# Kernel tuning notes

Hardware: AMD Instinct MI355X
Metric: run time of the kernel (lower is better)

## Reference

```python
import jax, jax.numpy as jnp
import numpy as np

# dims: B batch, N nodes, E edges, C=dim_in, W=window_len, D=embed_dim, O=dim_out, K=link_len, NB=bootstrap count
B, N, E, C, W, D, O, K, NB = 16, 2000, 3000, 17, 12, 16, 256, 3, 3


def setup_inputs() -> dict:
    key = jax.random.key(0)
    ks = jax.random.split(key, 20)
    return {
        "x": jax.random.normal(ks[0], (B, N, C), jnp.float32),
        "x_window": jax.random.normal(ks[1], (B, W, N, 1), jnp.float32),
        "node_embeddings": jax.random.normal(ks[2], (N, D), jnp.float32) * 0.1,
        "fixed_adj": 0,
        "adj": jax.random.normal(ks[3], (N, N), jnp.float32),
        "stay_cost": 1,
        "jump_cost": 1,
        "ZFC_input": jax.random.normal(ks[4], (B, O // 8), jnp.float32),
        "hodge_Laplacian": jax.random.normal(ks[5], (E, E), jnp.float32) * 0.02,
        "x_e_window": jax.random.normal(ks[6], (B, W, E, 1), jnp.float32),
        "incidence_matrix": jax.random.normal(ks[7], (N, E), jnp.float32) * 0.02,
        "weights_pool": jax.random.normal(ks[8], (D, K, C, O // 4), jnp.float32) * 0.05,
        "window_weights_supra": jax.random.normal(ks[9], (D, 1, O // 8), jnp.float32) * 0.05,
        "window_weights_temporal": jax.random.normal(ks[10], (D, 1, O // 2), jnp.float32) * 0.05,
        "bias_pool": jax.random.normal(ks[11], (D, O), jnp.float32) * 0.05,
        "T_param": jax.random.normal(ks[12], (W,), jnp.float32) * 0.1,
        "lin_w": jax.random.normal(ks[13], (1, 1), jnp.float32),
        "lin_b": jax.random.normal(ks[14], (1,), jnp.float32),
        "gnn_w": jax.random.normal(ks[15], (N, N), jnp.float32) * 0.02,
        "gnn_b": jnp.zeros((N,), jnp.float32),
        "bootstrap_idx": jnp.sort(jax.random.randint(ks[16], (NB,), 0, W)),
    }


def _forward(x, x_window, ne, fixed_adj, adj, stay_cost, jump_cost, ZFC_input,
             hodge, x_e_window, inc, wp, wws_p, wwt_p, bp, Tp, lin_w, lin_b,
             gnn_w, gnn_b, bidx):
    n = ne.shape[0]
    e = hodge.shape[0]
    b = x.shape[0]
    nb = bidx.shape[0]

    # adaptive transition matrix S (diag filled with stay_cost after relu)
    S0 = jax.nn.relu(ne @ ne.T)
    ii = jnp.arange(n)
    S0 = S0.at[ii, ii].set(jnp.float32(stay_cost))
    if fixed_adj:  # static Python bool branch
        S = adj * jnp.exp(S0)
    else:
        S = jax.nn.softmax(S0, axis=1)
    # faithful to torch broadcasting: column j divided by row-sum of row j
    S = S / jnp.sum(S, axis=1)

    # diffusion support power series: [I, S, S@S, ...]
    sup = [jnp.eye(n, dtype=S.dtype), S]
    for _ in range(2, K):
        sup.append(S @ sup[-1])
    supports = jnp.stack(sup, axis=0)  # (K, N, N)

    # supra-Laplacian: hodge on diagonal blocks, jump_cost*I on strict upper blocks
    supra = (jnp.kron(jnp.eye(nb, dtype=hodge.dtype), hodge)
             + jnp.kron(jnp.triu(jnp.ones((nb, nb), hodge.dtype), 1),
                        jnp.float32(jump_cost) * jnp.eye(e, dtype=hodge.dtype)))  # (nb*E, nb*E)

    # adaptive weights/bias from node embeddings
    weights = jnp.einsum('nd,dkio->nkio', ne, wp)   # (N, K, C, O/4)
    bias = ne @ bp                                   # (N, O)

    # graph diffusion branch
    x_s = jnp.einsum('knm,bmc->bknc', supports, x).transpose(0, 2, 1, 3)  # (B,N,K,C)
    x_sconv = jnp.einsum('bnki,nkio->bno', x_s, weights)                   # (B,N,O/4)

    # supra / hypergraph branch
    wws = jnp.einsum('nd,dio->nio', ne, wws_p)                 # (N,1,O/8)
    xe = x_e_window[:, bidx].reshape(b, nb * e, 1)             # bootstrap gather
    xe = xe * lin_w[0, 0] + lin_b[0]                           # Linear(1,1)
    xes = jnp.einsum('bmi,mn->bni', xe, supra).reshape(b, nb, 1, e)
    xen = jnp.einsum('bfim,mn->bfin', xes, inc.T).reshape(b, nb, n, 1)
    x_e_n_wconv = jnp.einsum('bfni,nio->bfno', xen, wws).mean(axis=1)  # (B,N,O/8)

    # temporal window branch (einsum fuses the permute + matmul with T)
    wwt = jnp.einsum('nd,dio->nio', ne, wwt_p)                  # (N,1,O/2)
    x_wconv_t = jnp.einsum('btni,nio,t->bno', x_window, wwt, Tp)  # (B,N,O/2)

    # ZFC branch: repeat over nodes, GNN = Linear(N,N) + relu, reshape (view) back
    ZFC = jnp.tile(ZFC_input.reshape(b, -1, 1), (1, 1, n))      # (B,O/8,N)
    zout = jax.nn.relu(ZFC @ gnn_w.T + gnn_b)                   # (B,O/8,N)
    x_ZFC = zout.reshape(b, n, -1)                              # (B,N,O/8) (reshape, not transpose)

    return jnp.concatenate([x_sconv, x_ZFC, x_wconv_t, x_e_n_wconv], axis=-1) + bias


def reference(x, x_window, node_embeddings, fixed_adj, adj, stay_cost, jump_cost,
              ZFC_input, hodge_Laplacian, x_e_window, incidence_matrix,
              weights_pool, window_weights_supra, window_weights_temporal,
              bias_pool, T_param, lin_w, lin_b, gnn_w, gnn_b, bootstrap_idx):
    return _forward(x, x_window, node_embeddings, fixed_adj, adj, stay_cost,
                    jump_cost, ZFC_input, hodge_Laplacian, x_e_window,
                    incidence_matrix, weights_pool, window_weights_supra,
                    window_weights_temporal, bias_pool, T_param, lin_w, lin_b,
                    gnn_w, gnn_b, bootstrap_idx)
```

## Files before the change

kernel.cpp:

```cpp
#include <hip/hip_runtime.h>
#include <hip/hip_bf16.h>

typedef __hip_bfloat16 bf16;
typedef unsigned short ushort_t;
typedef __attribute__((ext_vector_type(8))) short short8;
typedef __attribute__((ext_vector_type(4))) short short4_t;
typedef __attribute__((ext_vector_type(4))) float f32x4;
typedef __attribute__((ext_vector_type(2))) float f32x2;

#define B_ 16
#define N_ 2000
#define E_ 3000
#define C_ 17
#define W_ 12
#define D_ 16
#define O_ 256
#define NB_ 3
#define KPAD 2048
#define KI_ 51
#define SEGS 75
#define ECH 40
#define EPAD 768
#define JB 48

static __device__ __forceinline__ ushort_t f2b(float f) {
  bf16 h = __float2bfloat16(f);
  return *reinterpret_cast<ushort_t*>(&h);
}
static __device__ __forceinline__ float b2f_u(ushort_t u) {
  bf16 h = *reinterpret_cast<bf16*>(&u);
  return __bfloat162float(h);
}
__device__ __forceinline__ int idxval(const int* p, int i) {
  int iv = p[i];
  if (iv >= 0 && iv < 1000000) return iv;
  return (int)__int_as_float(iv);
}

__device__ __forceinline__ void mm_body(int bx, int by,
    const ushort_t* __restrict__ A, const ushort_t* __restrict__ BT,
    float* __restrict__ Cf, ushort_t* __restrict__ Cb, int writeCb,
    ushort_t* smem) {
  ushort_t (*lds)[4096] = (ushort_t(*)[4096])smem;
  const int t = threadIdx.x;
  const int m0 = bx * 16;
  const int j0 = by * JB;
  const int wv = t >> 6, lane = t & 63;
  const int lm = lane & 15, lg = lane >> 4;
  const char* gA = (const char*)A + (size_t)m0 * (KPAD*2);
  const char* gB = (const char*)BT + (size_t)j0 * (KPAD*2);

  f32x4 acc = {0.f,0.f,0.f,0.f};

  auto stage = [&](int p, int s) {
    const long kb = (long)s * 128;
#pragma unroll
    for (int u = 0; u < 2; ++u) {
      int x = (u*256 + t) << 4;
      int y = x ^ (((x >> 7) & 7) << 4);
      int r = y >> 7, c = y & 127;
      const char* gp = (r < 16) ? gA + (long)r*(KPAD*2) + kb + c
                                : gB + (long)(r-16)*(KPAD*2) + kb + c;
      __builtin_amdgcn_global_load_lds(
          (const __attribute__((address_space(1))) void*)gp,
          (__attribute__((address_space(3))) void*)(&lds[p][u*2048 + wv*512]),
          16, 0, 0);
    }
  };

  auto compute = [&](int p) {
    if (wv < 3) {
      const char* base = (const char*)&lds[p][0];
#pragma unroll
      for (int kg = 0; kg < 2; ++kg) {
        int xA = (lm << 7) + (kg << 6) + (lg << 4);
        xA ^= ((xA >> 7) & 7) << 4;
        short8 a = *(const short8*)(base + xA);
        int xB = ((16 + wv*16 + lm) << 7) + (kg << 6) + (lg << 4);
        xB ^= ((xB >> 7) & 7) << 4;
        short8 b = *(const short8*)(base + xB);
        acc = __builtin_amdgcn_mfma_f32_16x16x32_bf16(a, b, acc, 0, 0, 0);
      }
    }
  };

  stage(0, 0);
  stage(1, 1);
  for (int s = 0; s < 32; ++s) {
    int p = s % 3;
    if (s < 30) {
      stage((s + 2) % 3, s + 2);
      asm volatile("s_waitcnt vmcnt(4)" ::: "memory");
    } else if (s == 30) {
      asm volatile("s_waitcnt vmcnt(2)" ::: "memory");
    } else {
      asm volatile("s_waitcnt vmcnt(0)" ::: "memory");
    }
    __builtin_amdgcn_s_barrier();
    asm volatile("" ::: "memory");
    compute(p);
    asm volatile("" ::: "memory");
    __builtin_amdgcn_s_barrier();
  }

  if (wv < 3) {
    int j = j0 + wv*16 + lm;
    int m = m0 + lg*4;
    *(f32x4*)(Cf + (long)j*KPAD + m) = acc;
    if (writeCb) {
      short4_t hv;
#pragma unroll
      for (int q = 0; q < 4; ++q)
        hv[q] = (m + q < N_) ? (short)f2b(acc[q]) : (short)0;
      *(short4_t*)(Cb + (long)j*KPAD + m) = hv;
    }
  }
}

__device__ __forceinline__ void hodge_body(int w, const float* __restrict__ u,
    const float* __restrict__ hodge, float* __restrict__ xesP, float* ul) {
  const int t = threadIdx.x;
  const int e2 = (w % 12)*256 + t;
  const int seg = w / 12;
  const int e1a = seg*ECH;
  for (int idx = t; idx < ECH*16; idx += 256) {
    int bb = idx / ECH, ee = idx - bb*ECH;
    ul[ee*16 + bb] = u[bb*E_ + e1a + ee];
  }
  __syncthreads();
  if (e2 >= E_) return;
  float acc[16] = {};
  for (int ee = 0; ee < ECH; ee += 8) {
    float h[8];
#pragma unroll
    for (int q = 0; q < 8; ++q) h[q] = hodge[(long)(e1a + ee + q)*E_ + e2];
#pragma unroll
    for (int q = 0; q < 8; ++q) {
#pragma unroll
      for (int g4 = 0; g4 < 4; ++g4) {
        f32x4 u4 = *(const f32x4*)&ul[(ee + q)*16 + g4*4];
        acc[g4*4+0] += u4.x*h[q];
        acc[g4*4+1] += u4.y*h[q];
        acc[g4*4+2] += u4.z*h[q];
        acc[g4*4+3] += u4.w*h[q];
      }
    }
  }
#pragma unroll
  for (int bb = 0; bb < 16; ++bb)
    xesP[((long)seg*16 + bb)*E_ + e2] = acc[bb];
}

__global__ __launch_bounds__(256) void k_pre(
    const float* __restrict__ xew, const int* __restrict__ bidx,
    const float* __restrict__ lw, const float* __restrict__ lb,
    const int* __restrict__ jc, float* __restrict__ u, float* __restrict__ v,
    const float* __restrict__ xwin, const float* __restrict__ Tp,
    float* __restrict__ xw, const float* __restrict__ gw, float* __restrict__ g,
    const float* __restrict__ x, ushort_t* __restrict__ BT1,
    const float* __restrict__ ne, const float* __restrict__ wp,
    const float* __restrict__ bp, ushort_t* __restrict__ Wd,
    const int* __restrict__ stay, ushort_t* __restrict__ S) {
  __shared__ float smem[10248];
  const int bid = blockIdx.x;
  const int t = threadIdx.x;
  if (bid < 188) {
    int idx = bid*256 + t;
    if (idx >= B_*E_) return;
    int b = idx / E_, e = idx - b*E_;
    const float lwf = lw[0], lbf = lb[0];
    float uu = 0.f, vv = 0.f;
#pragma unroll
    for (int f = 0; f < NB_; ++f) {
      int tt = idxval(bidx, f);
      if (tt < 0) tt = 0;
      if (tt >= W_) tt = W_ - 1;
      float val = xew[(b*W_ + tt)*E_ + e]*lwf + lbf;
      uu += val;
      vv += (float)(NB_ - 1 - f)*val;
    }
    u[idx] = uu;
    v[idx] = vv*(float)(*jc);
  } else if (bid < 313) {
    int idx = (bid - 188)*256 + t;
    int b = idx / N_, n = idx - b*N_;
    float s = 0.f;
#pragma unroll
    for (int tt = 0; tt < W_; ++tt) s += xwin[(b*W_ + tt)*N_ + n]*Tp[tt];
    xw[idx] = s;
  } else if (bid < 2313) {
    int i = bid - 313;
    float* red = smem;
    float s = 0.f;
    for (int j4 = t*4; j4 < N_; j4 += 1024) {
      f32x4 vv = *(const f32x4*)(gw + (long)i*N_ + j4);
      s += vv.x + vv.y + vv.z + vv.w;
    }
#pragma unroll
    for (int off = 32; off > 0; off >>= 1) s += __shfl_xor(s, off, 64);
    if ((t & 63) == 0) red[t >> 6] = s;
    __syncthreads();
    if (t == 0) g[i] = red[0] + red[1] + red[2] + red[3];
  } else if (bid < 2601) {
    int j = bid - 2313;
    int bb = j / C_, cc = j - bb*C_;
#pragma unroll
    for (int uu = 0; uu < 8; ++uu) {
      int n = t + uu*256;
      float vv = 0.f;
      if (bb < B_ && n < N_) vv = x[(bb*N_ + n)*C_ + cc];
      BT1[(long)j*KPAD + n] = f2b(vv);
    }
  } else if (bid < 3251) {
    float (*wp_l)[256] = (float(*)[256])smem;
    float (*ne_l)[16]  = (float(*)[16])(smem + 4096);
    int w = bid - 2601;
    int c0 = (w % 13) * 256;
    int n0 = (w / 13) * 40;
    int c = c0 + t;
    int ki = c >> 6, o = c & 63;
#pragma unroll
    for (int d = 0; d < 16; ++d)
      wp_l[d][t] = (ki < KI_) ? wp[d*3264 + c] : bp[d*256 + o];
    for (int i = t; i < 40*16; i += 256)
      ne_l[i >> 4][i & 15] = ne[(long)(n0 + (i >> 4))*16 + (i & 15)];
    __syncthreads();
    float wreg[16];
#pragma unroll
    for (int d = 0; d < 16; ++d) wreg[d] = wp_l[d][t];
    ushort_t* wout = Wd + (long)n0*3328 + c;
    for (int n = 0; n < 40; ++n) {
      f32x4 a4 = {0.f,0.f,0.f,0.f};
#pragma unroll
      for (int q = 0; q < 4; ++q) {
        f32x4 nv = *(const f32x4*)&ne_l[n][q*4];
        a4.x += nv.x*wreg[q*4+0];
        a4.y += nv.y*wreg[q*4+1];
        a4.z += nv.z*wreg[q*4+2];
        a4.w += nv.w*wreg[q*4+3];
      }
      wout[(long)n*3328] = f2b(a4.x + a4.y + a4.z + a4.w);
    }
  } else {
    float* ne_l = smem;
    float* reds = smem + 10240;
    float* reds2 = smem + 10244;
    const int i = bid - 3251;
    const int i2 = i + 1024;
    const bool has2 = (i2 < N_);
    f32x4 nei[4], nei2[4];
#pragma unroll
    for (int q = 0; q < 4; ++q) {
      nei[q] = *(const f32x4*)(ne + i*16 + q*4);
      nei2[q] = has2 ? *(const f32x4*)(ne + (long)i2*16 + q*4) : (f32x4){0.f,0.f,0.f,0.f};
    }
    const float stayf = (float)(*stay);
    float vals[8], vals2[8];
    float s = 0.f, s2 = 0.f;
    for (int c = 0; c < 4; ++c) {
      __syncthreads();
#pragma unroll
      for (int uu = 0; uu < 8; ++uu) {
        int unit = t + uu*256;
        int row = unit >> 2, dq = unit & 3;
        int gj = c*512 + row;
        f32x4 vv = {0.f,0.f,0.f,0.f};
        if (gj < N_) vv = *(const f32x4*)(ne + (long)gj*16 + dq*4);
        *(f32x4*)(ne_l + row*20 + dq*4) = vv;
      }
      __syncthreads();
#pragma unroll
      for (int r = 0; r < 2; ++r) {
        int row_l = t + r*256;
        int j = c*512 + row_l;
        float e = 0.f, e2 = 0.f;
        if (j < N_) {
          f32x4 a4 = {0.f,0.f,0.f,0.f}, b4 = {0.f,0.f,0.f,0.f};
#pragma unroll
          for (int q = 0; q < 4; ++q) {
            f32x4 nl = *(const f32x4*)(ne_l + row_l*20 + q*4);
            a4 += nei[q]*nl;
            b4 += nei2[q]*nl;
          }
          float dot = a4.x + a4.y + a4.z + a4.w;
          float vv = dot > 0.f ? dot : 0.f;
          if (j == i) vv = stayf;
          e = __expf(vv);
          s += e;
          if (has2) {
            float dot2 = b4.x + b4.y + b4.z + b4.w;
            float v2 = dot2 > 0.f ? dot2 : 0.f;
            if (j == i2) v2 = stayf;
            e2 = __expf(v2);
            s2 += e2;
          }
        }
        vals[2*c + r] = e;
        vals2[2*c + r] = e2;
      }
    }
#pragma unroll
    for (int off = 32; off > 0; off >>= 1) {
      s  += __shfl_xor(s,  off, 64);
      s2 += __shfl_xor(s2, off, 64);
    }
    if ((t & 63) == 0) { reds[t >> 6] = s; reds2[t >> 6] = s2; }
    __syncthreads();
    s  = reds[0] + reds[1] + reds[2] + reds[3];
    s2 = reds2[0] + reds2[1] + reds2[2] + reds2[3];
    const float inv = 1.f/s;
    const float inv2 = has2 ? 1.f/s2 : 0.f;
#pragma unroll
    for (int it = 0; it < 8; ++it) {
      int j = t + it*256;
      S[(long)i*KPAD + j] = f2b(vals[it]*inv);
      S[(long)i2*KPAD + j] = has2 ? f2b(vals2[it]*inv2) : (ushort_t)0;
    }
  }
}

__global__ __launch_bounds__(256) void k_mmh(const ushort_t* __restrict__ A,
    const ushort_t* __restrict__ BT1, float* __restrict__ C32a,
    ushort_t* __restrict__ BT2,
    const float* __restrict__ u, const float* __restrict__ hodge,
    float* __restrict__ xesP) {
  __shared__ ushort_t smem[3*4096];
  const int bid = blockIdx.x;
  if (bid < 768) mm_body(bid & 127, bid >> 7, A, BT1, C32a, BT2, 1, smem);
  else           hodge_body(bid - 768, u, hodge, xesP, (float*)smem);
}

__global__ __launch_bounds__(256) void k_mmr(const ushort_t* __restrict__ A,
    const ushort_t* __restrict__ BT2, float* __restrict__ C32b,
    const float* __restrict__ xesP, const float* __restrict__ v,
    float* __restrict__ xes) {
  __shared__ ushort_t smem[3*4096];
  const int bid = blockIdx.x;
  if (bid < 768) {
    mm_body(bid & 127, bid >> 7, A, BT2, C32b, nullptr, 0, smem);
  } else {
    int idx = (bid - 768)*256 + threadIdx.x;
    if (idx >= B_*E_) return;
    int b = idx / E_, e = idx - b*E_;
    float s = v[idx];
#pragma unroll 15
    for (int q = 0; q < SEGS; ++q) s += xesP[((long)q*16 + b)*E_ + e];
    xes[idx] = s;
  }
}

__global__ __launch_bounds__(256) void k_inc(const float* __restrict__ xes,
                                             const float* __restrict__ inc,
                                             float* __restrict__ xenP) {
  __shared__ float xes_l[16*EPAD];
  const int t = threadIdx.x;
  const int wv = t >> 6, lane = t & 63;
  const int cy = blockIdx.y;
  const int n0 = blockIdx.x*8;
  for (int i4 = t; i4 < 16*(EPAD/4); i4 += 256) {
    int row = i4 / (EPAD/4);
    int el = (i4 - row*(EPAD/4)) << 2;
    int e = cy*EPAD + el;
    f32x4 vv = {0.f,0.f,0.f,0.f};
    if (e < E_) vv = *(const f32x4*)(xes + (long)row*E_ + e);
    *(f32x4*)&xes_l[row*EPAD + el] = vv;
  }
  __syncthreads();
  const int na = n0 + wv*2;
  const int nb = na + 1;
  const float* rowA = inc + (long)na*E_ + cy*EPAD;
  const float* rowB = inc + (long)nb*E_ + cy*EPAD;
  float accA[16] = {}, accB[16] = {};
#pragma unroll
  for (int g = 0; g < 3; ++g) {
    int e4 = (g*64 + lane) << 2;
    bool ok = (cy*EPAD + e4) < E_;
    f32x4 ia = {0.f,0.f,0.f,0.f}, ib = {0.f,0.f,0.f,0.f};
    if (ok) { ia = *(const f32x4*)(rowA + e4); ib = *(const f32x4*)(rowB + e4); }
#pragma unroll
    for (int b = 0; b < 16; ++b) {
      f32x4 xs = *(const f32x4*)&xes_l[b*EPAD + e4];
      accA[b] += xs.x*ia.x + xs.y*ia.y + xs.z*ia.z + xs.w*ia.w;
      accB[b] += xs.x*ib.x + xs.y*ib.y + xs.z*ib.z + xs.w*ib.w;
    }
  }
#pragma unroll
  for (int b = 0; b < 16; ++b) {
#pragma unroll
    for (int off = 32; off > 0; off >>= 1) {
      accA[b] += __shfl_xor(accA[b], off, 64);
      accB[b] += __shfl_xor(accB[b], off, 64);
    }
  }
  const int bl = lane & 15;
  float oA = 0.f, oB = 0.f;
#pragma unroll
  for (int b = 0; b < 16; ++b)
    if (bl == b) { oA = accA[b]; oB = accB[b]; }
  if (lane < 16)
    xenP[((long)cy*16 + bl)*N_ + na] = oA*(1.f/3.f);
  else if (lane < 32)
    xenP[((long)cy*16 + bl)*N_ + nb] = oB*(1.f/3.f);
}

#define NT2 2
__global__ __launch_bounds__(256) void k_tailF(const float* __restrict__ x,
                          const float* __restrict__ C32a,
                          const float* __restrict__ C32b,
                          const ushort_t* __restrict__ Wd,
                          const float* __restrict__ ne,
                          const float* __restrict__ bp,
                          const float* __restrict__ wwt, const float* __restrict__ wws,
                          const float* __restrict__ zfc, const float* __restrict__ gnnb,
                          const float* __restrict__ g, const float* __restrict__ xw,
                          const float* __restrict__ xenP,
                          float* __restrict__ out) {
  __shared__ float xs_l[52*20];
  __shared__ float ne_l[NT2][16];
  __shared__ float wb[NT2][160];
  __shared__ float bi[NT2][192];
  __shared__ float gi_l[NT2][32], gb_l[NT2][32];
  __shared__ int   q_l[NT2][32];
  __shared__ float zf_l[16*32];
  __shared__ float xwv[16][NT2], xev[16][NT2];
  const int t = threadIdx.x;
  if (blockIdx.x < 2000) {
    const int n = blockIdx.x;
    const int lane = t & 63, wv = t >> 6;
    for (int idx = t; idx < KI_*16; idx += 256) {
      int ki = idx >> 4, b = idx & 15;
      int k = ki / C_, cc = ki - k*C_;
      float v;
      if (k == 0)      v = x[(b*N_ + n)*C_ + cc];
      else if (k == 1) v = C32a[(long)(b*C_ + cc)*KPAD + n];
      else             v = C32b[(long)(b*C_ + cc)*KPAD + n];
      xs_l[ki*20 + b] = v;
    }
    if (t < 16) xs_l[KI_*20 + t] = 1.0f;
    __syncthreads();
    const ushort_t* wrow = Wd + (long)n*3328 + lane;
    f32x4 acc = {0.f,0.f,0.f,0.f};
#pragma unroll
    for (int ki = 0; ki < 52; ++ki) {
      float w = b2f_u(wrow[ki*64]);
      f32x4 xs4 = *(const f32x4*)&xs_l[ki*20 + wv*4];
      acc += xs4 * w;
    }
#pragma unroll
    for (int j = 0; j < 4; ++j)
      out[((long)((wv*4 + j)*N_ + n))*O_ + lane] = acc[j];
  } else {
    const int n0 = (blockIdx.x - 2000)*NT2;
    zf_l[t] = zfc[t];
    zf_l[t + 256] = zfc[t + 256];
    if (t < NT2*16) ne_l[t >> 4][t & 15] = ne[(n0 + (t >> 4))*16 + (t & 15)];
    if (t < NT2*32) {
      int nl = t >> 5, j = t & 31;
      int flat = (n0 + nl)*32 + j;
      int q = flat / N_;
      int i = flat - q*N_;
      q_l[nl][j] = q;
      gi_l[nl][j] = g[i];
      gb_l[nl][j] = gnnb[i];
    }
    if (t < 16*NT2) {
      int b = t / NT2, nl = t - b*NT2;
      int n = n0 + nl;
      xwv[b][nl] = xw[b*N_ + n];
      xev[b][nl] = xenP[b*N_ + n] + xenP[(16 + b)*N_ + n]
                 + xenP[(32 + b)*N_ + n] + xenP[(48 + b)*N_ + n];
    }
    __syncthreads();
    for (int idx = t; idx < NT2*192; idx += 256) {
      int nl = idx / 192, op = idx - nl*192;
      float wv2 = 0.f, bv = 0.f;
#pragma unroll
      for (int d = 0; d < 16; ++d) {
        float nd = ne_l[nl][d];
        bv += nd * bp[d*256 + 64 + op];
        float ww = 0.f;
        if (op >= 32 && op < 160) ww = wwt[d*128 + (op - 32)];
        else if (op >= 160)       ww = wws[d*32 + (op - 160)];
        wv2 += nd * ww;
      }
      bi[nl][op] = bv;
      if (op >= 32) wb[nl][op - 32] = wv2;
    }
    __syncthreads();
    for (int idx = t; idx < 16*NT2*192; idx += 256) {
      int b = idx / (NT2*192);
      int r = idx - b*(NT2*192);
      int nl = r / 192, op = r - nl*192;
      float val;
      if (op < 32) {
        float z = zf_l[b*32 + q_l[nl][op]]*gi_l[nl][op] + gb_l[nl][op];
        val = z > 0.f ? z : 0.f;
      } else if (op < 160) {
        val = xwv[b][nl] * wb[nl][op - 32];
      } else {
        val = xev[b][nl] * wb[nl][op - 32];
      }
      out[((long)(b*N_ + n0 + nl))*O_ + 64 + op] = val + bi[nl][op];
    }
  }
}

extern "C" void kernel_launch(void* const* d_in, const int* in_sizes, int n_in,
                              void* d_out, int out_size, void* d_ws, size_t ws_size,
                              hipStream_t stream) {
  const float* x     = (const float*)d_in[0];
  const float* xwin  = (const float*)d_in[1];
  const float* ne    = (const float*)d_in[2];
  const int*   stay  = (const int*)d_in[5];
  const int*   jc    = (const int*)d_in[6];
  const float* zfc   = (const float*)d_in[7];
  const float* hodge = (const float*)d_in[8];
  const float* xew   = (const float*)d_in[9];
  const float* inc   = (const float*)d_in[10];
  const float* wp    = (const float*)d_in[11];
  const float* wws   = (const float*)d_in[12];
  const float* wwt   = (const float*)d_in[13];
  const float* bp    = (const float*)d_in[14];
  const float* Tp    = (const float*)d_in[15];
  const float* lw    = (const float*)d_in[16];
  const float* lb    = (const float*)d_in[17];
  const float* gw    = (const float*)d_in[18];
  const float* gnnb  = (const float*)d_in[19];
  const int*   bidx  = (const int*)d_in[20];
  float* out = (float*)d_out;

  char* wsb = (char*)d_ws;
  float*    C32a = (float*)(wsb);
  float*    C32b = (float*)(wsb + 2359296);
  ushort_t* BT1  = (ushort_t*)(wsb + 2359296);
  float* u    = (float*)(wsb + 4718592);
  float* v    = (float*)(wsb + 4910592);
  float* xes  = (float*)(wsb + 5102592);
  float* xw   = (float*)(wsb + 5294592);
  float* g    = (float*)(wsb + 5422592);
  float* xenP = (float*)(wsb + 5430592);
  ushort_t* Wd = (ushort_t*)(wsb + 5942592);

  char* ob = (char*)d_out;
  ushort_t* S    = (ushort_t*)(ob);
  ushort_t* BT2  = (ushort_t*)(ob + 8388608);
  float*    xesP = (float*)(ob + 9568256);

  k_pre<<<4275, 256, 0, stream>>>(xew, bidx, lw, lb, jc, u, v,
                                  xwin, Tp, xw, gw, g, x, BT1,
                                  ne, wp, bp, Wd, stay, S);
  k_mmh<<<1668, 256, 0, stream>>>(S, BT1, C32a, BT2, u, hodge, xesP);
  k_mmr<<<956, 256, 0, stream>>>(S, BT2, C32b, xesP, v, xes);
  k_inc<<<dim3(250, 4), 256, 0, stream>>>(xes, inc, xenP);
  k_tailF<<<3000, 256, 0, stream>>>(x, C32a, C32b, Wd, ne, bp, wwt, wws,
                                    zfc, gnnb, g, xw, xenP, out);
}
```

Before: 251.0 us.

## Restructure S-matmul to full-K LDS A tile and move hodge into pre-kernel

The matmul body now loads an entire 16x2048 A row-block into LDS once and has each wave stream its own 16-column B tile straight from global memory over the whole K range. This replaces the triple-buffered per-K-step staging with barriers, and all four waves now compute instead of three. The hodge-Laplacian partial products move into the pre-kernel, which computes the bootstrap sum u inline, so the u buffer and the mixed matmul/hodge kernel go away. The trade-offs are much larger LDS use per block, which lowers occupancy, and B reads that bypass LDS; the pre-kernel also gets longer.

```diff
diff --git a/kernel.cpp b/kernel.cpp
--- a/kernel.cpp
+++ b/kernel.cpp
@@ -21,7 +21,6 @@
 #define SEGS 75
 #define ECH 40
 #define EPAD 768
-#define JB 48
 
 static __device__ __forceinline__ ushort_t f2b(float f) {
   bf16 h = __float2bfloat16(f);
@@ -37,74 +36,43 @@
   return (int)__int_as_float(iv);
 }
 
-__device__ __forceinline__ void mm_body(int bx, int by,
+__device__ __forceinline__ void mm_body4(int bx, int by,
     const ushort_t* __restrict__ A, const ushort_t* __restrict__ BT,
     float* __restrict__ Cf, ushort_t* __restrict__ Cb, int writeCb,
-    ushort_t* smem) {
-  ushort_t (*lds)[4096] = (ushort_t(*)[4096])smem;
+    ushort_t* smem ) {
   const int t = threadIdx.x;
   const int m0 = bx * 16;
-  const int j0 = by * JB;
   const int wv = t >> 6, lane = t & 63;
   const int lm = lane & 15, lg = lane >> 4;
-  const char* gA = (const char*)A + (size_t)m0 * (KPAD*2);
-  const char* gB = (const char*)BT + (size_t)j0 * (KPAD*2);
-
-  f32x4 acc = {0.f,0.f,0.f,0.f};
-
-  auto stage = [&](int p, int s) {
-    const long kb = (long)s * 128;
-#pragma unroll
-    for (int u = 0; u < 2; ++u) {
-      int x = (u*256 + t) << 4;
-      int y = x ^ (((x >> 7) & 7) << 4);
-      int r = y >> 7, c = y & 127;
-      const char* gp = (r < 16) ? gA + (long)r*(KPAD*2) + kb + c
-                                : gB + (long)(r-16)*(KPAD*2) + kb + c;
-      __builtin_amdgcn_global_load_lds(
-          (const __attribute__((address_space(1))) void*)gp,
-          (__attribute__((address_space(3))) void*)(&lds[p][u*2048 + wv*512]),
-          16, 0, 0);
-    }
-  };
-
-  auto compute = [&](int p) {
-    if (wv < 3) {
-      const char* base = (const char*)&lds[p][0];
-#pragma unroll
-      for (int kg = 0; kg < 2; ++kg) {
-        int xA = (lm << 7) + (kg << 6) + (lg << 4);
-        xA ^= ((xA >> 7) & 7) << 4;
-        short8 a = *(const short8*)(base + xA);
-        int xB = ((16 + wv*16 + lm) << 7) + (kg << 6) + (lg << 4);
-        xB ^= ((xB >> 7) & 7) << 4;
-        short8 b = *(const short8*)(base + xB);
-        acc = __builtin_amdgcn_mfma_f32_16x16x32_bf16(a, b, acc, 0, 0, 0);
-      }
-    }
-  };
-
-  stage(0, 0);
-  stage(1, 1);
-  for (int s = 0; s < 32; ++s) {
-    int p = s % 3;
-    if (s < 30) {
-      stage((s + 2) % 3, s + 2);
-      asm volatile("s_waitcnt vmcnt(4)" ::: "memory");
-    } else if (s == 30) {
-      asm volatile("s_waitcnt vmcnt(2)" ::: "memory");
-    } else {
-      asm volatile("s_waitcnt vmcnt(0)" ::: "memory");
-    }
-    __builtin_amdgcn_s_barrier();
-    asm volatile("" ::: "memory");
-    compute(p);
-    asm volatile("" ::: "memory");
-    __builtin_amdgcn_s_barrier();
-  }
-
-  if (wv < 3) {
-    int j = j0 + wv*16 + lm;
+  const int jt = by*4 + wv;
+  const char* gA = (const char*)A + (size_t)m0 * 4096;
+
+#pragma unroll
+  for (int u = 0; u < 16; ++u) {
+    int x = (u*256 + t) << 4;
+    int y = x ^ (((x >> 12) & 7) << 4);
+    const char* gp = gA + (size_t)(y >> 12)*4096 + (y & 4095);
+    __builtin_amdgcn_global_load_lds(
+        (const __attribute__((address_space(1))) void*)gp,
+        (__attribute__((address_space(3))) void*)(smem + (((u*256 + wv*64)) << 3)),
+        16, 0, 0);
+  }
+  asm volatile("s_waitcnt vmcnt(0)" ::: "memory");
+  __builtin_amdgcn_s_barrier();
+
+  if (jt < 18) {
+    const char* base = (const char*)smem;
+    const char* gB = (const char*)BT + (size_t)(jt*16 + lm)*4096 + lg*16;
+    f32x4 acc = {0.f,0.f,0.f,0.f};
+#pragma unroll 8
+    for (int kg = 0; kg < 64; ++kg) {
+      int la = (lm << 12) + (kg << 6) + (lg << 4);
+      int pa = la ^ ((lm & 7) << 4);
+      short8 a = *(const short8*)(base + pa);
+      short8 b = *(const short8*)(gB + kg*64);
+      acc = __builtin_amdgcn_mfma_f32_16x16x32_bf16(a, b, acc, 0, 0, 0);
+    }
+    int j = jt*16 + lm;
     int m = m0 + lg*4;
     *(f32x4*)(Cf + (long)j*KPAD + m) = acc;
     if (writeCb) {
@@ -117,50 +85,17 @@
   }
 }
 
-__device__ __forceinline__ void hodge_body(int w, const float* __restrict__ u,
-    const float* __restrict__ hodge, float* __restrict__ xesP, float* ul) {
-  const int t = threadIdx.x;
-  const int e2 = (w % 12)*256 + t;
-  const int seg = w / 12;
-  const int e1a = seg*ECH;
-  for (int idx = t; idx < ECH*16; idx += 256) {
-    int bb = idx / ECH, ee = idx - bb*ECH;
-    ul[ee*16 + bb] = u[bb*E_ + e1a + ee];
-  }
-  __syncthreads();
-  if (e2 >= E_) return;
-  float acc[16] = {};
-  for (int ee = 0; ee < ECH; ee += 8) {
-    float h[8];
-#pragma unroll
-    for (int q = 0; q < 8; ++q) h[q] = hodge[(long)(e1a + ee + q)*E_ + e2];
-#pragma unroll
-    for (int q = 0; q < 8; ++q) {
-#pragma unroll
-      for (int g4 = 0; g4 < 4; ++g4) {
-        f32x4 u4 = *(const f32x4*)&ul[(ee + q)*16 + g4*4];
-        acc[g4*4+0] += u4.x*h[q];
-        acc[g4*4+1] += u4.y*h[q];
-        acc[g4*4+2] += u4.z*h[q];
-        acc[g4*4+3] += u4.w*h[q];
-      }
-    }
-  }
-#pragma unroll
-  for (int bb = 0; bb < 16; ++bb)
-    xesP[((long)seg*16 + bb)*E_ + e2] = acc[bb];
-}
-
 __global__ __launch_bounds__(256) void k_pre(
     const float* __restrict__ xew, const int* __restrict__ bidx,
     const float* __restrict__ lw, const float* __restrict__ lb,
-    const int* __restrict__ jc, float* __restrict__ u, float* __restrict__ v,
+    const int* __restrict__ jc, float* __restrict__ v,
     const float* __restrict__ xwin, const float* __restrict__ Tp,
     float* __restrict__ xw, const float* __restrict__ gw, float* __restrict__ g,
     const float* __restrict__ x, ushort_t* __restrict__ BT1,
     const float* __restrict__ ne, const float* __restrict__ wp,
     const float* __restrict__ bp, ushort_t* __restrict__ Wd,
-    const int* __restrict__ stay, ushort_t* __restrict__ S) {
+    const int* __restrict__ stay, ushort_t* __restrict__ S,
+    const float* __restrict__ hodge, float* __restrict__ xesP) {
   __shared__ float smem[10248];
   const int bid = blockIdx.x;
   const int t = threadIdx.x;
@@ -169,17 +104,15 @@
     if (idx >= B_*E_) return;
     int b = idx / E_, e = idx - b*E_;
     const float lwf = lw[0], lbf = lb[0];
-    float uu = 0.f, vv = 0.f;
+    float vv = 0.f;
 #pragma unroll
     for (int f = 0; f < NB_; ++f) {
       int tt = idxval(bidx, f);
       if (tt < 0) tt = 0;
       if (tt >= W_) tt = W_ - 1;
       float val = xew[(b*W_ + tt)*E_ + e]*lwf + lbf;
-      uu += val;
       vv += (float)(NB_ - 1 - f)*val;
     }
-    u[idx] = uu;
     v[idx] = vv*(float)(*jc);
   } else if (bid < 313) {
     int idx = (bid - 188)*256 + t;
@@ -241,7 +174,7 @@
       }
       wout[(long)n*3328] = f2b(a4.x + a4.y + a4.z + a4.w);
     }
-  } else {
+  } else if (bid < 4275) {
     float* ne_l = smem;
     float* reds = smem + 10240;
     float* reds2 = smem + 10244;
@@ -316,30 +249,68 @@
       S[(long)i*KPAD + j] = f2b(vals[it]*inv);
       S[(long)i2*KPAD + j] = has2 ? f2b(vals2[it]*inv2) : (ushort_t)0;
     }
-  }
-}
-
-__global__ __launch_bounds__(256) void k_mmh(const ushort_t* __restrict__ A,
+  } else {
+    float* ul = smem;
+    const int w = bid - 4275;
+    const int e2 = (w % 12)*256 + t;
+    const int seg = w / 12;
+    const int e1a = seg*ECH;
+    const float lwf = lw[0], lbf = lb[0];
+    for (int idx = t; idx < ECH*16; idx += 256) {
+      int bb = idx / ECH, ee = idx - bb*ECH;
+      int e1 = e1a + ee;
+      float uu = 0.f;
+#pragma unroll
+      for (int f = 0; f < NB_; ++f) {
+        int tt = idxval(bidx, f);
+        if (tt < 0) tt = 0;
+        if (tt >= W_) tt = W_ - 1;
+        uu += xew[(bb*W_ + tt)*E_ + e1]*lwf + lbf;
+      }
+      ul[ee*16 + bb] = uu;
+    }
+    __syncthreads();
+    if (e2 >= E_) return;
+    float acc[16] = {};
+    for (int ee = 0; ee < ECH; ee += 8) {
+      float h[8];
+#pragma unroll
+      for (int q = 0; q < 8; ++q) h[q] = hodge[(long)(e1a + ee + q)*E_ + e2];
+#pragma unroll
+      for (int q = 0; q < 8; ++q) {
+#pragma unroll
+        for (int g4 = 0; g4 < 4; ++g4) {
+          f32x4 u4 = *(const f32x4*)&ul[(ee + q)*16 + g4*4];
+          acc[g4*4+0] += u4.x*h[q];
+          acc[g4*4+1] += u4.y*h[q];
+          acc[g4*4+2] += u4.z*h[q];
+          acc[g4*4+3] += u4.w*h[q];
+        }
+      }
+    }
+#pragma unroll
+    for (int bb = 0; bb < 16; ++bb)
+      xesP[((long)seg*16 + bb)*E_ + e2] = acc[bb];
+  }
+}
+
+__global__ __launch_bounds__(256) void k_mm1(const ushort_t* __restrict__ A,
     const ushort_t* __restrict__ BT1, float* __restrict__ C32a,
-    ushort_t* __restrict__ BT2,
-    const float* __restrict__ u, const float* __restrict__ hodge,
-    float* __restrict__ xesP) {
-  __shared__ ushort_t smem[3*4096];
-  const int bid = blockIdx.x;
-  if (bid < 768) mm_body(bid & 127, bid >> 7, A, BT1, C32a, BT2, 1, smem);
-  else           hodge_body(bid - 768, u, hodge, xesP, (float*)smem);
+    ushort_t* __restrict__ BT2) {
+  __shared__ ushort_t smem[32768];
+  mm_body4(blockIdx.x, blockIdx.y, A, BT1, C32a, BT2, 1, smem);
 }
 
 __global__ __launch_bounds__(256) void k_mmr(const ushort_t* __restrict__ A,
     const ushort_t* __restrict__ BT2, float* __restrict__ C32b,
     const float* __restrict__ xesP, const float* __restrict__ v,
     float* __restrict__ xes) {
-  __shared__ ushort_t smem[3*4096];
+  __shared__ ushort_t smem[32768];
   const int bid = blockIdx.x;
-  if (bid < 768) {
-    mm_body(bid & 127, bid >> 7, A, BT2, C32b, nullptr, 0, smem);
+  if (bid < 640) {
+    mm_body4(bid & 127, bid >> 7, A, BT2, C32b, nullptr, 0, smem);
   } else {
-    int idx = (bid - 768)*256 + threadIdx.x;
+    int idx = (bid - 640)*256 + threadIdx.x;
     if (idx >= B_*E_) return;
     int b = idx / E_, e = idx - b*E_;
     float s = v[idx];
@@ -533,7 +504,6 @@
   float*    C32a = (float*)(wsb);
   float*    C32b = (float*)(wsb + 2359296);
   ushort_t* BT1  = (ushort_t*)(wsb + 2359296);
-  float* u    = (float*)(wsb + 4718592);
   float* v    = (float*)(wsb + 4910592);
   float* xes  = (float*)(wsb + 5102592);
   float* xw   = (float*)(wsb + 5294592);
@@ -546,11 +516,11 @@
   ushort_t* BT2  = (ushort_t*)(ob + 8388608);
   float*    xesP = (float*)(ob + 9568256);
 
-  k_pre<<<4275, 256, 0, stream>>>(xew, bidx, lw, lb, jc, u, v,
+  k_pre<<<5175, 256, 0, stream>>>(xew, bidx, lw, lb, jc, v,
                                   xwin, Tp, xw, gw, g, x, BT1,
-                                  ne, wp, bp, Wd, stay, S);
-  k_mmh<<<1668, 256, 0, stream>>>(S, BT1, C32a, BT2, u, hodge, xesP);
-  k_mmr<<<956, 256, 0, stream>>>(S, BT2, C32b, xesP, v, xes);
+                                  ne, wp, bp, Wd, stay, S, hodge, xesP);
+  k_mm1<<<dim3(128,5), 256, 0, stream>>>(S, BT1, C32a, BT2);
+  k_mmr<<<828, 256, 0, stream>>>(S, BT2, C32b, xesP, v, xes);
   k_inc<<<dim3(250, 4), 256, 0, stream>>>(xes, inc, xenP);
   k_tailF<<<3000, 256, 0, stream>>>(x, C32a, C32b, Wd, ne, bp, wwt, wws,
                                     zfc, gnnb, g, xw, xenP, out);
```

Result: slower. 275.3 us (+9.7%).
